# Performance work log

Hardware: AMD Instinct MI355X
Metric: run time of the kernel (lower is better)

## Reference

```python
import jax, jax.numpy as jnp
import numpy as np

P_DIM, M_DIM = 512, 768
PROJ, HID, NCLS = 512, 256, 2
EPS = 1e-5


def _bn_eval(x, g, b):
    # BatchNorm1d in eval mode with fresh buffers: running_mean=0, running_var=1
    return x / jnp.sqrt(1.0 + EPS) * g + b


def setup_inputs() -> dict:
    key = jax.random.key(0)
    ks = jax.random.split(key, 8)
    x = jax.random.normal(ks[0], (256, P_DIM + M_DIM), dtype=jnp.float32)
    W1 = jax.random.normal(ks[1], (PROJ, P_DIM * M_DIM), dtype=jnp.float32) * 0.002
    b1 = jnp.zeros((PROJ,), jnp.float32)
    ln_g = jnp.ones((PROJ,), jnp.float32)
    ln_b = jnp.zeros((PROJ,), jnp.float32)
    W2 = jax.random.normal(ks[2], (HID, PROJ), dtype=jnp.float32) * 0.04
    b2 = jnp.zeros((HID,), jnp.float32)
    bn1_g = jnp.ones((HID,), jnp.float32)
    bn1_b = jnp.zeros((HID,), jnp.float32)
    W3 = jax.random.normal(ks[3], (HID // 2, HID), dtype=jnp.float32) * 0.06
    b3 = jnp.zeros((HID // 2,), jnp.float32)
    bn2_g = jnp.ones((HID // 2,), jnp.float32)
    bn2_b = jnp.zeros((HID // 2,), jnp.float32)
    W4 = jax.random.normal(ks[4], (NCLS, HID // 2), dtype=jnp.float32) * 0.09
    b4 = jnp.zeros((NCLS,), jnp.float32)
    return dict(x=x, W1=W1, b1=b1, ln_g=ln_g, ln_b=ln_b, W2=W2, b2=b2,
                bn1_g=bn1_g, bn1_b=bn1_b, W3=W3, b3=b3,
                bn2_g=bn2_g, bn2_b=bn2_b, W4=W4, b4=b4)


def reference(x, W1, b1, ln_g, ln_b, W2, b2, bn1_g, bn1_b, W3, b3, bn2_g, bn2_b, W4, b4):
    p = x[:, :P_DIM]                     # [B, P]
    m = x[:, P_DIM:P_DIM + M_DIM]        # [B, M]
    # kron[b, i*M + j] = p[b,i]*m[b,j]; Linear(kron_flat) fused into one contraction
    W1r = W1.reshape(PROJ, P_DIM, M_DIM)
    fused = jnp.einsum('bp,bm,kpm->bk', p, m, W1r) + b1   # [B, PROJ]
    # LayerNorm + ReLU (dropout is identity in eval)
    mu = jnp.mean(fused, axis=-1, keepdims=True)
    var = jnp.var(fused, axis=-1, keepdims=True)
    h = (fused - mu) / jnp.sqrt(var + EPS) * ln_g + ln_b
    h = jax.nn.relu(h)
    # classifier MLP with BatchNorm1d (eval-mode buffers)
    h = jax.nn.relu(_bn_eval(h @ W2.T + b2, bn1_g, bn1_b))
    h = jax.nn.relu(_bn_eval(h @ W3.T + b3, bn2_g, bn2_b))
    logits = h @ W4.T + b4               # [B, NCLS]
    return logits
```

## Files before the change

kernel.cpp:

```cpp
#include <hip/hip_runtime.h>
#include <hip/hip_bf16.h>

typedef __attribute__((ext_vector_type(4))) float f32x4;
typedef __attribute__((ext_vector_type(16))) float f32x16;
typedef __attribute__((ext_vector_type(8))) short short8;
typedef __attribute__((ext_vector_type(4))) short short4v;
typedef unsigned short ushort_t;

#define BATCH 256
#define PDIM 512
#define MDIM 768
#define XCOLS 1280
#define PROJ 512
#define HID 256
#define KTOT (PDIM * MDIM)

#define BN 32
#define NT 16
#define PSPLIT 32
#define PI_PER 16
#define NJW 12
#define NSTEPS 192

__device__ __forceinline__ ushort_t f2bf(float f) {
  __hip_bfloat16 h = __float2bfloat16(f);
  return __builtin_bit_cast(ushort_t, h);
}
__device__ __forceinline__ float bf2f(ushort_t u) {
  union { unsigned int i; float f; } c;
  c.i = ((unsigned int)u) << 16;
  return c.f;
}

__global__ void prep_kernel(const float* __restrict__ x, ushort_t* __restrict__ mF) {
  int tid = blockIdx.x * blockDim.x + threadIdx.x;
  int nth = gridDim.x * blockDim.x;
  for (int c = tid; c < NJW * 8 * 4 * 64; c += nth) {
    int lane = c & 63;
    int ks = (c >> 6) & 3;
    int mf = (c >> 8) & 7;
    int jw = c >> 11;
    int row = mf * 32 + (lane & 31);
    int k0 = jw * 64 + ks * 16 + ((lane >> 5) << 3);
    const float* src = x + row * XCOLS + PDIM + k0;
    f32x4 v0 = *(const f32x4*)src;
    f32x4 v1 = *(const f32x4*)(src + 4);
    short8 o;
#pragma unroll
    for (int i = 0; i < 4; ++i) {
      o[i] = (short)f2bf(v0[i]);
      o[i + 4] = (short)f2bf(v1[i]);
    }
    ((short8*)mF)[c] = o;
  }
}

__global__ __launch_bounds__(512, 4)
void einsum_kernel(const float* __restrict__ W1, const ushort_t* __restrict__ mF,
                   const float* __restrict__ x, float* __restrict__ outp,
                   int atomic_mode) {
  __shared__ ushort_t Bf[2][2048];
  __shared__ float pl[PI_PER * BATCH];

  const int ntile = blockIdx.x & 15;
  const int ps    = blockIdx.x >> 4;
  const int pi0   = ps * PI_PER;
  const int n0    = ntile * BN;
  const int t     = threadIdx.x;
  const int lane  = t & 63;
  const int w     = t >> 6;

  {
    const int b = t & 255, half = t >> 8;
    const float* xr = x + (size_t)b * XCOLS + pi0 + half * 8;
    f32x4 v0 = *(const f32x4*)xr;
    f32x4 v1 = *(const f32x4*)(xr + 4);
#pragma unroll
    for (int i = 0; i < 4; ++i) {
      pl[(half * 8 + i) * BATCH + b]     = v0[i];
      pl[(half * 8 + 4 + i) * BATCH + b] = v1[i];
    }
  }

  const int r = t >> 4, q2 = t & 15;
  const float* wrow = W1 + (size_t)(n0 + r) * KTOT + (size_t)pi0 * MDIM + q2 * 4;
  const int wb = (((q2 >> 2) * 64) + (((q2 >> 1) & 1) << 5) + r) * 16 + ((q2 & 1) << 3);

  const short8* mv = (const short8*)mF;
  const int mbase = w * 256 + lane;
  short8 ac0 = mv[mbase];
  short8 ac1 = mv[mbase + 64];
  short8 ac2 = mv[mbase + 128];
  short8 ac3 = mv[mbase + 192];

  f32x4 wv = __builtin_nontemporal_load((const f32x4*)wrow);
  f32x4 nv = __builtin_nontemporal_load((const f32x4*)(wrow + MDIM));

  f32x16 fa;
#pragma unroll
  for (int i = 0; i < 16; ++i) fa[i] = 0.f;

  __syncthreads();

  for (int s = 0; s < NSTEPS; ++s) {
    int s2 = s + 2; if (s2 >= NSTEPS) s2 -= NSTEPS;
    const int kk2 = (s2 & 15) * MDIM + (s2 >> 4) * 64;
    f32x4 xv = __builtin_nontemporal_load((const f32x4*)(wrow + kk2));

    {
      short4v o;
#pragma unroll
      for (int i = 0; i < 4; ++i) o[i] = (short)f2bf(wv[i]);
      *(short4v*)((char*)&Bf[s & 1][0] + wb) = o;
    }
    asm volatile("s_waitcnt lgkmcnt(0)" ::: "memory");
    __builtin_amdgcn_s_barrier();
    asm volatile("" ::: "memory");

    const short8* rb = (const short8*)&Bf[s & 1][0];
    const float pa = pl[(s & 15) * BATCH + w * 32 + (lane & 31)];

#define GENMM(ac, ks)                                                  \
    {                                                                  \
      short8 bv = rb[(ks) * 64 + lane];                                \
      short8 aA;                                                       \
      _Pragma("unroll")                                                \
      for (int e = 0; e < 8; ++e)                                      \
        aA[e] = (short)f2bf(pa * bf2f((ushort_t)ac[e]));               \
      fa = __builtin_amdgcn_mfma_f32_32x32x16_bf16(aA, bv, fa, 0, 0, 0); \
    }
    GENMM(ac0, 0)
    GENMM(ac1, 1)
    GENMM(ac2, 2)
    GENMM(ac3, 3)
#undef GENMM

    if ((s & 15) == 15) {
      int jn = (s >> 4) + 1; if (jn >= NJW) jn = 0;
      const short8* srcn = mv + jn * 2048 + mbase;
      ac0 = srcn[0];
      ac1 = srcn[64];
      ac2 = srcn[128];
      ac3 = srcn[192];
    }
    wv = nv; nv = xv;
  }

  const int col = n0 + (lane & 31);
  const int rb2 = w * 32 + ((lane >> 5) << 2);
  if (atomic_mode) {
#pragma unroll
    for (int rr = 0; rr < 16; ++rr) {
      int row = rb2 + (rr & 3) + ((rr >> 2) << 3);
      atomicAdd(&outp[(size_t)row * PROJ + col], fa[rr]);
    }
  } else {
    float* dst = outp + (size_t)ps * BATCH * PROJ;
#pragma unroll
    for (int rr = 0; rr < 16; ++rr) {
      int row = rb2 + (rr & 3) + ((rr >> 2) << 3);
      dst[(size_t)row * PROJ + col] = fa[rr];
    }
  }
}

__global__ __launch_bounds__(256)
void mlp_kernel(const float* __restrict__ part, int nps,
                const float* __restrict__ b1, const float* __restrict__ lng,
                const float* __restrict__ lnb, const float* __restrict__ W2,
                const float* __restrict__ b2, const float* __restrict__ g1,
                const float* __restrict__ bb1, const float* __restrict__ W3,
                const float* __restrict__ b3, const float* __restrict__ g2,
                const float* __restrict__ bb2, const float* __restrict__ W4,
                const float* __restrict__ b4, float* __restrict__ out) {
  __shared__ float h1[PROJ];
  __shared__ float h2[HID];
  __shared__ float h3[HID / 2];
  __shared__ float red[16];
  const int b = blockIdx.x, t = threadIdx.x;

  float f0 = 0.f, f1 = 0.f;
  const float* p0 = part + (size_t)b * PROJ + t;
#pragma unroll 4
  for (int s = 0; s < nps; ++s) {
    f0 += p0[0];
    f1 += p0[256];
    p0 += (size_t)BATCH * PROJ;
  }
  f0 += b1[t];
  f1 += b1[t + 256];

  float sum = f0 + f1, ss = f0 * f0 + f1 * f1;
#pragma unroll
  for (int o = 32; o > 0; o >>= 1) {
    sum += __shfl_xor(sum, o);
    ss  += __shfl_xor(ss, o);
  }
  const int wv = t >> 6, ln = t & 63;
  if (ln == 0) { red[wv] = sum; red[8 + wv] = ss; }
  __syncthreads();
  sum = red[0] + red[1] + red[2] + red[3];
  ss  = red[8] + red[9] + red[10] + red[11];
  float mu   = sum * (1.f / 512.f);
  float var  = ss * (1.f / 512.f) - mu * mu;
  float rstd = rsqrtf(var + 1e-5f);
  h1[t]       = fmaxf(0.f, (f0 - mu) * rstd * lng[t] + lnb[t]);
  h1[t + 256] = fmaxf(0.f, (f1 - mu) * rstd * lng[t + 256] + lnb[t + 256]);
  __syncthreads();

  const float bninv = rsqrtf(1.f + 1e-5f);
  {
    const f32x4* wr = (const f32x4*)(W2 + (size_t)t * PROJ);
    const f32x4* hv = (const f32x4*)h1;
    float a = 0.f;
#pragma unroll 4
    for (int i = 0; i < PROJ / 4; ++i) {
      f32x4 wq = wr[i], h = hv[i];
      a += wq[0] * h[0] + wq[1] * h[1] + wq[2] * h[2] + wq[3] * h[3];
    }
    h2[t] = fmaxf(0.f, (a + b2[t]) * bninv * g1[t] + bb1[t]);
  }
  __syncthreads();
  if (t < 128) {
    const f32x4* wr = (const f32x4*)(W3 + (size_t)t * HID);
    const f32x4* hv = (const f32x4*)h2;
    float a = 0.f;
#pragma unroll 4
    for (int i = 0; i < HID / 4; ++i) {
      f32x4 wq = wr[i], h = hv[i];
      a += wq[0] * h[0] + wq[1] * h[1] + wq[2] * h[2] + wq[3] * h[3];
    }
    h3[t] = fmaxf(0.f, (a + b3[t]) * bninv * g2[t] + bb2[t]);
  }
  __syncthreads();
  if (t < 2) {
    const float* wr = W4 + t * 128;
    float a = 0.f;
#pragma unroll 4
    for (int i = 0; i < 128; ++i) a += wr[i] * h3[i];
    out[b * 2 + t] = a + b4[t];
  }
}

extern "C" void kernel_launch(void* const* d_in, const int* in_sizes, int n_in,
                              void* d_out, int out_size, void* d_ws, size_t ws_size,
                              hipStream_t stream) {
  const float* x   = (const float*)d_in[0];
  const float* W1  = (const float*)d_in[1];
  const float* b1  = (const float*)d_in[2];
  const float* lng = (const float*)d_in[3];
  const float* lnb = (const float*)d_in[4];
  const float* W2  = (const float*)d_in[5];
  const float* b2  = (const float*)d_in[6];
  const float* g1  = (const float*)d_in[7];
  const float* bb1 = (const float*)d_in[8];
  const float* W3  = (const float*)d_in[9];
  const float* b3  = (const float*)d_in[10];
  const float* g2  = (const float*)d_in[11];
  const float* bb2 = (const float*)d_in[12];
  const float* W4  = (const float*)d_in[13];
  const float* b4  = (const float*)d_in[14];
  float* out = (float*)d_out;

  char* ws = (char*)d_ws;
  ushort_t* mF = (ushort_t*)ws;
  float* big   = (float*)(ws + 524288);

  size_t need = 524288 + (size_t)PSPLIT * BATCH * PROJ * 4;
  bool partial = ws_size >= need;

  hipLaunchKernelGGL(prep_kernel, dim3(256), dim3(256), 0, stream, x, mF);
  if (partial) {
    hipLaunchKernelGGL(einsum_kernel, dim3(NT * PSPLIT), dim3(512), 0, stream,
                       W1, mF, x, big, 0);
    hipLaunchKernelGGL(mlp_kernel, dim3(BATCH), dim3(256), 0, stream, big, PSPLIT,
                       b1, lng, lnb, W2, b2, g1, bb1, W3, b3, g2, bb2, W4, b4, out);
  } else {
    hipMemsetAsync(big, 0, (size_t)BATCH * PROJ * 4, stream);
    hipLaunchKernelGGL(einsum_kernel, dim3(NT * PSPLIT), dim3(512), 0, stream,
                       W1, mF, x, big, 1);
    hipLaunchKernelGGL(mlp_kernel, dim3(BATCH), dim3(256), 0, stream, big, 1,
                       b1, lng, lnb, W2, b2, g1, bb1, W3, b3, g2, bb2, W4, b4, out);
  }
}
```

Before: 235.0 us.

## Enlarge W1 staging tiles to cut barriers and swizzle LDS layout

Restructures the einsum main loop so each barrier step stages 256 K-elements of W1 per row (four rows per wave, contiguous 1KB loads) into a larger XOR-swizzled LDS double buffer. Each step then issues 16 MFMAs instead of 4, and the m-fragment register prefetch is interleaved mid-step. This aims to cut barrier count and per-step overhead and improve global load coalescing. The cost is much higher register use (16 short8 fragments) under the 512x4 launch bound, which risks spills or lower occupancy.

```diff
diff --git a/kernel.cpp b/kernel.cpp
--- a/kernel.cpp
+++ b/kernel.cpp
@@ -20,7 +20,7 @@
 #define PSPLIT 32
 #define PI_PER 16
 #define NJW 12
-#define NSTEPS 192
+#define NSS 48
 
 __device__ __forceinline__ ushort_t f2bf(float f) {
   __hip_bfloat16 h = __float2bfloat16(f);
@@ -59,7 +59,7 @@
 void einsum_kernel(const float* __restrict__ W1, const ushort_t* __restrict__ mF,
                    const float* __restrict__ x, float* __restrict__ outp,
                    int atomic_mode) {
-  __shared__ ushort_t Bf[2][2048];
+  __shared__ ushort_t Bs[2][8192];
   __shared__ float pl[PI_PER * BATCH];
 
   const int ntile = blockIdx.x & 15;
@@ -69,6 +69,7 @@
   const int t     = threadIdx.x;
   const int lane  = t & 63;
   const int w     = t >> 6;
+  const int hi    = lane >> 5;
 
   {
     const int b = t & 255, half = t >> 8;
@@ -82,19 +83,53 @@
     }
   }
 
-  const int r = t >> 4, q2 = t & 15;
-  const float* wrow = W1 + (size_t)(n0 + r) * KTOT + (size_t)pi0 * MDIM + q2 * 4;
-  const int wb = (((q2 >> 2) * 64) + (((q2 >> 1) & 1) << 5) + r) * 16 + ((q2 & 1) << 3);
+  const float* wq0 = W1 + (size_t)(n0 + w * 4 + 0) * KTOT + (size_t)pi0 * MDIM + lane * 4;
+  const float* wq1 = wq0 + (size_t)KTOT;
+  const float* wq2 = wq0 + 2 * (size_t)KTOT;
+  const float* wq3 = wq0 + 3 * (size_t)KTOT;
+
+  const int r0 = w * 4;
+  const int wb0 = ((r0 + 0) * 512 + lane * 8) ^ (((r0 + 0) & 7) << 4);
+  const int wb1 = ((r0 + 1) * 512 + lane * 8) ^ (((r0 + 1) & 7) << 4);
+  const int wb2 = ((r0 + 2) * 512 + lane * 8) ^ (((r0 + 2) & 7) << 4);
+  const int wb3 = ((r0 + 3) * 512 + lane * 8) ^ (((r0 + 3) & 7) << 4);
+
+  const int anchor = ((lane & 31) << 9) | (hi << 4);
+  const int swz    = (lane & 7) << 4;
 
   const short8* mv = (const short8*)mF;
-  const int mbase = w * 256 + lane;
-  short8 ac0 = mv[mbase];
-  short8 ac1 = mv[mbase + 64];
-  short8 ac2 = mv[mbase + 128];
-  short8 ac3 = mv[mbase + 192];
-
-  f32x4 wv = __builtin_nontemporal_load((const f32x4*)wrow);
-  f32x4 nv = __builtin_nontemporal_load((const f32x4*)(wrow + MDIM));
+  const int mb = w * 256 + lane;
+
+  short8 ac[16];
+#pragma unroll
+  for (int q = 0; q < 4; ++q)
+#pragma unroll
+    for (int k4 = 0; k4 < 4; ++k4)
+      ac[q * 4 + k4] = mv[q * 2048 + k4 * 64 + mb];
+
+  f32x4 c0 = __builtin_nontemporal_load((const f32x4*)wq0);
+  f32x4 c1 = __builtin_nontemporal_load((const f32x4*)wq1);
+  f32x4 c2 = __builtin_nontemporal_load((const f32x4*)wq2);
+  f32x4 c3 = __builtin_nontemporal_load((const f32x4*)wq3);
+  {
+    short4v o0, o1, o2, o3;
+#pragma unroll
+    for (int i = 0; i < 4; ++i) {
+      o0[i] = (short)f2bf(c0[i]);
+      o1[i] = (short)f2bf(c1[i]);
+      o2[i] = (short)f2bf(c2[i]);
+      o3[i] = (short)f2bf(c3[i]);
+    }
+    char* bw = (char*)&Bs[0][0];
+    *(short4v*)(bw + wb0) = o0;
+    *(short4v*)(bw + wb1) = o1;
+    *(short4v*)(bw + wb2) = o2;
+    *(short4v*)(bw + wb3) = o3;
+  }
+  c0 = __builtin_nontemporal_load((const f32x4*)(wq0 + 256));
+  c1 = __builtin_nontemporal_load((const f32x4*)(wq1 + 256));
+  c2 = __builtin_nontemporal_load((const f32x4*)(wq2 + 256));
+  c3 = __builtin_nontemporal_load((const f32x4*)(wq3 + 256));
 
   f32x16 fa;
 #pragma unroll
@@ -102,52 +137,70 @@
 
   __syncthreads();
 
-  for (int s = 0; s < NSTEPS; ++s) {
-    int s2 = s + 2; if (s2 >= NSTEPS) s2 -= NSTEPS;
-    const int kk2 = (s2 & 15) * MDIM + (s2 >> 4) * 64;
-    f32x4 xv = __builtin_nontemporal_load((const f32x4*)(wrow + kk2));
-
-    {
-      short4v o;
-#pragma unroll
-      for (int i = 0; i < 4; ++i) o[i] = (short)f2bf(wv[i]);
-      *(short4v*)((char*)&Bf[s & 1][0] + wb) = o;
-    }
-    asm volatile("s_waitcnt lgkmcnt(0)" ::: "memory");
-    __builtin_amdgcn_s_barrier();
-    asm volatile("" ::: "memory");
-
-    const short8* rb = (const short8*)&Bf[s & 1][0];
-    const float pa = pl[(s & 15) * BATCH + w * 32 + (lane & 31)];
-
-#define GENMM(ac, ks)                                                  \
-    {                                                                  \
-      short8 bv = rb[(ks) * 64 + lane];                                \
-      short8 aA;                                                       \
-      _Pragma("unroll")                                                \
-      for (int e = 0; e < 8; ++e)                                      \
-        aA[e] = (short)f2bf(pa * bf2f((ushort_t)ac[e]));               \
-      fa = __builtin_amdgcn_mfma_f32_32x32x16_bf16(aA, bv, fa, 0, 0, 0); \
-    }
-    GENMM(ac0, 0)
-    GENMM(ac1, 1)
-    GENMM(ac2, 2)
-    GENMM(ac3, 3)
-#undef GENMM
-
-    if ((s & 15) == 15) {
-      int jn = (s >> 4) + 1; if (jn >= NJW) jn = 0;
-      const short8* srcn = mv + jn * 2048 + mbase;
-      ac0 = srcn[0];
-      ac1 = srcn[64];
-      ac2 = srcn[128];
-      ac3 = srcn[192];
-    }
-    wv = nv; nv = xv;
-  }
+  int koff2 = 512;
+  int jw2 = 0, pil = 0;
+
+#define KSROUND(KS)                                                          \
+  {                                                                          \
+    short8 bv = *(const short8*)(bsp + ((anchor + ((KS) << 5)) ^ swz));      \
+    short8 aA;                                                               \
+    _Pragma("unroll")                                                        \
+    for (int e = 0; e < 8; ++e)                                              \
+      aA[e] = (short)f2bf(pa * bf2f((ushort_t)ac[KS][e]));                   \
+    fa = __builtin_amdgcn_mfma_f32_32x32x16_bf16(aA, bv, fa, 0, 0, 0);       \
+  }
+
+#define BODY(P)                                                              \
+  {                                                                          \
+    const float pa = pl[pil * BATCH + (w << 5) + (lane & 31)];               \
+    const char* bsp = (const char*)&Bs[P][0];                                \
+    KSROUND(0) KSROUND(1) KSROUND(2) KSROUND(3)                              \
+    KSROUND(4) KSROUND(5) KSROUND(6) KSROUND(7)                              \
+    const int jw2n = (jw2 == 2) ? 0 : jw2 + 1;                               \
+    const short8* mq = mv + jw2n * 8192 + mb;                                \
+    _Pragma("unroll")                                                        \
+    for (int jq = 0; jq < 8; ++jq)                                           \
+      ac[jq] = mq[(jq >> 2) * 2048 + (jq & 3) * 64];                         \
+    KSROUND(8) KSROUND(9) KSROUND(10) KSROUND(11)                            \
+    KSROUND(12) KSROUND(13) KSROUND(14) KSROUND(15)                          \
+    _Pragma("unroll")                                                        \
+    for (int jq = 0; jq < 8; ++jq)                                           \
+      ac[8 + jq] = mq[4096 + (jq >> 2) * 2048 + (jq & 3) * 64];              \
+    {                                            \
+      short4v o0, o1, o2, o3;                                                \
+      _Pragma("unroll")                                                      \
+      for (int i = 0; i < 4; ++i) {                                          \
+        o0[i] = (short)f2bf(c0[i]);                                          \
+        o1[i] = (short)f2bf(c1[i]);                                          \
+        o2[i] = (short)f2bf(c2[i]);                                          \
+        o3[i] = (short)f2bf(c3[i]);                                          \
+      }                                                                      \
+      char* bw = (char*)&Bs[P ^ 1][0];                                       \
+      *(short4v*)(bw + wb0) = o0;                                            \
+      *(short4v*)(bw + wb1) = o1;                                            \
+      *(short4v*)(bw + wb2) = o2;                                            \
+      *(short4v*)(bw + wb3) = o3;                                            \
+    }                                                                        \
+    c0 = __builtin_nontemporal_load((const f32x4*)(wq0 + koff2));            \
+    c1 = __builtin_nontemporal_load((const f32x4*)(wq1 + koff2));            \
+    c2 = __builtin_nontemporal_load((const f32x4*)(wq2 + koff2));            \
+    c3 = __builtin_nontemporal_load((const f32x4*)(wq3 + koff2));            \
+    koff2 += 256; if (koff2 == 12288) koff2 = 0;                             \
+    asm volatile("s_waitcnt lgkmcnt(0)" ::: "memory");                       \
+    __builtin_amdgcn_s_barrier();                                            \
+    asm volatile("" ::: "memory");                                           \
+    jw2 = jw2n; if (jw2 == 0) ++pil;                                         \
+  }
+
+  for (int s2 = 0; s2 < NSS / 2; ++s2) {
+    BODY(0)
+    BODY(1)
+  }
+#undef BODY
+#undef KSROUND
 
   const int col = n0 + (lane & 31);
-  const int rb2 = w * 32 + ((lane >> 5) << 2);
+  const int rb2 = w * 32 + (hi << 2);
   if (atomic_mode) {
 #pragma unroll
     for (int rr = 0; rr < 16; ++rr) {
```

New measurement: 384.0 us. 1.63x slower.

## Stream W1 tiles directly into LDS via global_load_lds with triple buffering

Applied to the files above, without the earlier changes.

Replaces register-staged W1 loads (global load, convert to bf16, write to LDS) with direct global-to-LDS async loads of fp32 tiles into a 3-deep ring buffer with XOR swizzling. Each wave then reads fp32 B fragments from LDS and converts to bf16 just before the MFMA. This is meant to cut VGPR pressure and hide the HBM latency of the dominant W1 stream, at the cost of doubled LDS footprint and read bandwidth plus per-use conversion.

```diff
diff --git a/kernel.cpp b/kernel.cpp
--- a/kernel.cpp
+++ b/kernel.cpp
@@ -4,7 +4,6 @@
 typedef __attribute__((ext_vector_type(4))) float f32x4;
 typedef __attribute__((ext_vector_type(16))) float f32x16;
 typedef __attribute__((ext_vector_type(8))) short short8;
-typedef __attribute__((ext_vector_type(4))) short short4v;
 typedef unsigned short ushort_t;
 
 #define BATCH 256
@@ -59,7 +58,7 @@
 void einsum_kernel(const float* __restrict__ W1, const ushort_t* __restrict__ mF,
                    const float* __restrict__ x, float* __restrict__ outp,
                    int atomic_mode) {
-  __shared__ ushort_t Bf[2][2048];
+  __shared__ __align__(16) char Bs[3][8192];
   __shared__ float pl[PI_PER * BATCH];
 
   const int ntile = blockIdx.x & 15;
@@ -69,6 +68,7 @@
   const int t     = threadIdx.x;
   const int lane  = t & 63;
   const int w     = t >> 6;
+  const int hi    = lane >> 5;
 
   {
     const int b = t & 255, half = t >> 8;
@@ -82,9 +82,13 @@
     }
   }
 
-  const int r = t >> 4, q2 = t & 15;
-  const float* wrow = W1 + (size_t)(n0 + r) * KTOT + (size_t)pi0 * MDIM + q2 * 4;
-  const int wb = (((q2 >> 2) * 64) + (((q2 >> 1) & 1) << 5) + r) * 16 + ((q2 & 1) << 3);
+  const int wr = 4 * w + (lane >> 4);
+  const int wo = ((lane & 15) << 4) ^ ((wr & 15) << 4);
+  const char* wsrc = (const char*)(W1 + (size_t)(n0 + wr) * KTOT + (size_t)pi0 * MDIM) + wo;
+
+  const int r256 = (lane & 31) << 8;
+  const int sz_  = (lane & 15) << 4;
+  const int hi32 = hi << 5;
 
   const short8* mv = (const short8*)mF;
   const int mbase = w * 256 + lane;
@@ -93,8 +97,12 @@
   short8 ac2 = mv[mbase + 128];
   short8 ac3 = mv[mbase + 192];
 
-  f32x4 wv = __builtin_nontemporal_load((const f32x4*)wrow);
-  f32x4 nv = __builtin_nontemporal_load((const f32x4*)(wrow + MDIM));
+#define KOFFB(s) (((((s) & 15) * MDIM) + (((s) >> 4) * 64)) * 4)
+
+  __builtin_amdgcn_global_load_lds((const unsigned int*)(wsrc + KOFFB(0)),
+                                   (unsigned int*)(&Bs[0][0] + (w << 10)), 16, 0, 0);
+  __builtin_amdgcn_global_load_lds((const unsigned int*)(wsrc + KOFFB(1)),
+                                   (unsigned int*)(&Bs[1][0] + (w << 10)), 16, 0, 0);
 
   f32x16 fa;
 #pragma unroll
@@ -103,31 +111,37 @@
   __syncthreads();
 
   for (int s = 0; s < NSTEPS; ++s) {
-    int s2 = s + 2; if (s2 >= NSTEPS) s2 -= NSTEPS;
-    const int kk2 = (s2 & 15) * MDIM + (s2 >> 4) * 64;
-    f32x4 xv = __builtin_nontemporal_load((const f32x4*)(wrow + kk2));
-
-    {
-      short4v o;
-#pragma unroll
-      for (int i = 0; i < 4; ++i) o[i] = (short)f2bf(wv[i]);
-      *(short4v*)((char*)&Bf[s & 1][0] + wb) = o;
-    }
+    asm volatile("s_waitcnt vmcnt(1)" ::: "memory");
     asm volatile("s_waitcnt lgkmcnt(0)" ::: "memory");
+    __builtin_amdgcn_sched_barrier(0);
     __builtin_amdgcn_s_barrier();
     asm volatile("" ::: "memory");
 
-    const short8* rb = (const short8*)&Bf[s & 1][0];
-    const float pa = pl[(s & 15) * BATCH + w * 32 + (lane & 31)];
-
-#define GENMM(ac, ks)                                                  \
-    {                                                                  \
-      short8 bv = rb[(ks) * 64 + lane];                                \
-      short8 aA;                                                       \
-      _Pragma("unroll")                                                \
-      for (int e = 0; e < 8; ++e)                                      \
-        aA[e] = (short)f2bf(pa * bf2f((ushort_t)ac[e]));               \
-      fa = __builtin_amdgcn_mfma_f32_32x32x16_bf16(aA, bv, fa, 0, 0, 0); \
+    {
+      int s2 = s + 2; if (s2 >= NSTEPS) s2 -= NSTEPS;
+      const int b2 = s2 % 3;
+      __builtin_amdgcn_global_load_lds((const unsigned int*)(wsrc + KOFFB(s2)),
+                                       (unsigned int*)(&Bs[b2][0] + (w << 10)), 16, 0, 0);
+    }
+
+    const char* bsp = &Bs[s % 3][0];
+    const float pa = pl[(s & 15) * BATCH + (w << 5) + (lane & 31)];
+
+#define GENMM(AC, KS)                                                      \
+    {                                                                      \
+      const int kb = (KS) * 64 + hi32;                                     \
+      f32x4 b0 = *(const f32x4*)(bsp + r256 + ((kb) ^ sz_));               \
+      f32x4 b1 = *(const f32x4*)(bsp + r256 + ((kb + 16) ^ sz_));          \
+      short8 bvh, aA;                                                      \
+      _Pragma("unroll")                                                    \
+      for (int i2 = 0; i2 < 4; ++i2) {                                     \
+        bvh[i2]     = (short)f2bf(b0[i2]);                                 \
+        bvh[4 + i2] = (short)f2bf(b1[i2]);                                 \
+      }                                                                    \
+      _Pragma("unroll")                                                    \
+      for (int e = 0; e < 8; ++e)                                          \
+        aA[e] = (short)f2bf(pa * bf2f((ushort_t)AC[e]));                   \
+      fa = __builtin_amdgcn_mfma_f32_32x32x16_bf16(aA, bvh, fa, 0, 0, 0);  \
     }
     GENMM(ac0, 0)
     GENMM(ac1, 1)
@@ -143,11 +157,12 @@
       ac2 = srcn[128];
       ac3 = srcn[192];
     }
-    wv = nv; nv = xv;
-  }
+  }
+#undef KOFFB
+  asm volatile("s_waitcnt vmcnt(0)" ::: "memory");
 
   const int col = n0 + (lane & 31);
-  const int rb2 = w * 32 + ((lane >> 5) << 2);
+  const int rb2 = w * 32 + (hi << 2);
   if (atomic_mode) {
 #pragma unroll
     for (int rr = 0; rr < 16; ++rr) {
```

Result: slower. 298.2 us (+26.9%).
